# Optimization experiments

Measured on AMD Instinct MI355X. Metric: run time of the kernel, lower is better.

The kernel has to match this reference:

```python
import jax, jax.numpy as jnp
import numpy as np

B, T, S, D, V = 8, 128, 400, 512, 50000
EPS_LN = 1e-6

def setup_inputs() -> dict:
    key = jax.random.key(0)
    ks = jax.random.split(key, 10)
    a = jax.random.uniform(ks[0], (B, T, S), dtype=jnp.float32)
    attn_weights = a / jnp.sum(a, axis=-1, keepdims=True)  # row-stochastic like softmax attention
    return {
        'x': jax.random.normal(ks[1], (B, T, D), dtype=jnp.float32),
        'x_t': jax.random.normal(ks[2], (B, T, D), dtype=jnp.float32),
        'memory': jax.random.normal(ks[3], (B, S, D), dtype=jnp.float32),
        'attn_weights': attn_weights,
        'src': jax.random.randint(ks[4], (B, S), 0, V),
        'norm_a': jnp.ones((D,), jnp.float32),
        'norm_b': jnp.zeros((D,), jnp.float32),
        'proj_w': jax.random.normal(ks[5], (V, D), dtype=jnp.float32) * (1.0 / np.sqrt(D)),
        'proj_b': jnp.zeros((V,), jnp.float32),
        'wh_w': jax.random.normal(ks[6], (1, D), dtype=jnp.float32) * (1.0 / np.sqrt(D)),
        'wh_b': jnp.zeros((1,), jnp.float32),
        'ws_w': jax.random.normal(ks[7], (1, D), dtype=jnp.float32) * (1.0 / np.sqrt(D)),
        'ws_b': jnp.zeros((1,), jnp.float32),
        'wx_w': jax.random.normal(ks[8], (1, D), dtype=jnp.float32) * (1.0 / np.sqrt(D)),
        'wx_b': jnp.zeros((1,), jnp.float32),
        'bptr': jnp.zeros((1, 1), jnp.float32),
    }

def _layer_norm(x, a, b):
    mu = jnp.mean(x, axis=-1, keepdims=True)
    sd = jnp.std(x, axis=-1, keepdims=True)
    return a * (x - mu) / (sd + EPS_LN) + b

def reference(x, x_t, memory, attn_weights, src, norm_a, norm_b, proj_w, proj_b,
              wh_w, wh_b, ws_w, ws_b, wx_w, wx_b, bptr):
    # generation distribution over vocab: [B,T,V]
    dec_dist = jnp.einsum('btd,vd->btv', _layer_norm(x, norm_a, norm_b), proj_w) + proj_b
    # context vector h_t = attn @ memory: [B,T,D]
    h_t = jnp.einsum('bts,bsd->btd', attn_weights, memory)
    # p_gen gate: [B,T,1]
    logits = (jnp.einsum('btd,od->bto', h_t, wh_w) + wh_b
              + jnp.einsum('btd,od->bto', x, ws_w) + ws_b
              + jnp.einsum('btd,od->bto', x_t, wx_w) + wx_b
              + bptr[0, 0])
    p_gen = jax.nn.sigmoid(logits)
    # copy distribution via scatter_add of attention mass onto source token ids
    b_idx = jnp.arange(B)[:, None, None]
    t_idx = jnp.arange(T)[None, :, None]
    v_idx = src[:, None, :]  # broadcast over T -> [B,T,S] index
    enc_attn_dist = jnp.zeros((B, T, V), dtype=dec_dist.dtype).at[b_idx, t_idx, v_idx].add(attn_weights)
    out = jnp.log(p_gen * jax.nn.softmax(dec_dist, axis=-1) + (1.0 - p_gen) * enc_attn_dist + 1e-12)
    return out, p_gen
```

## Files before the change

### kernel.cpp

```cpp
#include <hip/hip_runtime.h>
#include <hip/hip_bf16.h>
#include <cstdint>

#define B_  8
#define T_  128
#define S_  400
#define D_  512
#define V_  50000
#define M_  (B_*T_)
#define NT_ 391
#define EPS_LN 1e-6f

typedef __bf16 bf16x8 __attribute__((ext_vector_type(8)));
typedef float  f32x4  __attribute__((ext_vector_type(4)));
typedef unsigned short u16;
typedef unsigned short u16x8 __attribute__((ext_vector_type(8)));

__device__ __forceinline__ float bf2f(u16 u) {
    union { unsigned i; float f; } c; c.i = ((unsigned)u) << 16; return c.f;
}
__device__ __forceinline__ u16 f2bf(float f) {
    union { float f; unsigned i; } c; c.f = f;
    unsigned i = c.i;
    unsigned r = (i + 0x7FFFu + ((i >> 16) & 1u)) >> 16;
    return (u16)r;
}

__device__ __forceinline__ float bsum(float v, float* sb) {
    #pragma unroll
    for (int o = 32; o; o >>= 1) v += __shfl_xor(v, o);
    __syncthreads();
    if ((threadIdx.x & 63) == 0) sb[threadIdx.x >> 6] = v;
    __syncthreads();
    return sb[0] + sb[1] + sb[2] + sb[3];
}

__global__ void k_mw(const float* __restrict__ mem, const float* __restrict__ wh,
                     float* __restrict__ mw) {
    __shared__ float sb[4];
    int row = blockIdx.x;
    const float* mr = mem + (size_t)row * D_;
    int t = threadIdx.x;
    float2 m2 = *(const float2*)(mr + t * 2);
    float2 w2 = *(const float2*)(wh + t * 2);
    float v = m2.x * w2.x + m2.y * w2.y;
    float tot = bsum(v, sb);
    if (t == 0) mw[row] = tot;
}

__global__ void k_wconv(const float* __restrict__ w, u16* __restrict__ wb) {
    size_t i = ((size_t)blockIdx.x * 256 + threadIdx.x) * 8;
    float4 a = *(const float4*)(w + i);
    float4 b = *(const float4*)(w + i + 4);
    u16x8 o;
    o[0] = f2bf(a.x); o[1] = f2bf(a.y); o[2] = f2bf(a.z); o[3] = f2bf(a.w);
    o[4] = f2bf(b.x); o[5] = f2bf(b.y); o[6] = f2bf(b.z); o[7] = f2bf(b.w);
    *(u16x8*)(wb + i) = o;
}

__global__ void k_rows(const float* __restrict__ x, const float* __restrict__ xt,
                       const float* __restrict__ attn, const float* __restrict__ mw,
                       const float* __restrict__ na, const float* __restrict__ nb,
                       const float* __restrict__ wsw, const float* __restrict__ wxw,
                       const float* __restrict__ whb, const float* __restrict__ wsb,
                       const float* __restrict__ wxb, const float* __restrict__ bp,
                       u16* __restrict__ Ab, float* __restrict__ pgen,
                       float* __restrict__ outp) {
    __shared__ float sb[4];
    int row = blockIdx.x;
    int b = row / T_;
    int tid = threadIdx.x;
    const float* xr  = x  + (size_t)row * D_;
    const float* xtr = xt + (size_t)row * D_;
    float2 xv = *(const float2*)(xr + tid * 2);
    float tsx  = bsum(xv.x + xv.y, sb);
    float tsx2 = bsum(xv.x * xv.x + xv.y * xv.y, sb);
    float mu  = tsx / (float)D_;
    float var = fmaxf(tsx2 / (float)D_ - mu * mu, 0.f);
    float rs  = 1.f / (sqrtf(var) + EPS_LN);
    float2 nav = *(const float2*)(na + tid * 2);
    float2 nbv = *(const float2*)(nb + tid * 2);
    u16 a0 = f2bf(nav.x * (xv.x - mu) * rs + nbv.x);
    u16 a1 = f2bf(nav.y * (xv.y - mu) * rs + nbv.y);
    ((unsigned*)(Ab + (size_t)row * D_))[tid] = (unsigned)a0 | ((unsigned)a1 << 16);
    float2 wsv = *(const float2*)(wsw + tid * 2);
    float2 wxv = *(const float2*)(wxw + tid * 2);
    float2 xtv = *(const float2*)(xtr + tid * 2);
    float dot = xv.x * wsv.x + xv.y * wsv.y + xtv.x * wxv.x + xtv.y * wxv.y;
    if (tid < 200) {
        const float* ar  = attn + (size_t)row * S_;
        const float* mwb = mw + b * S_;
        float2 av = *(const float2*)(ar + tid * 2);
        float2 mv = *(const float2*)(mwb + tid * 2);
        dot += av.x * mv.x + av.y * mv.y;
    }
    float tdot = bsum(dot, sb);
    if (tid == 0) {
        float logit = tdot + whb[0] + wsb[0] + wxb[0] + bp[0];
        float p = 1.f / (1.f + __expf(-logit));
        pgen[row] = p;
        outp[row] = p;
    }
}

__global__ __launch_bounds__(256) void k_gemm(const u16* __restrict__ Ab,
                                              const u16* __restrict__ Wb,
                                              const float* __restrict__ projb,
                                              u16* __restrict__ dec,
                                              float* __restrict__ psum) {
    __shared__ __align__(16) char smem[49152];
    int bid = blockIdx.x;
    int xcd = bid & 7, loc = bid >> 3;
    int wg = xcd * NT_ + loc;
    int mt = wg & 7, nt = wg >> 3;
    int brow = mt * 128, bcol = nt * 128;
    int tid = threadIdx.x, lane = tid & 63, wv = tid >> 6;
    int wm = wv >> 1, wn = wv & 1;
    int kq = lane >> 4, lr = lane & 15;

    size_t aoff[2], boff[2];
    int flatoff[2];
    #pragma unroll
    for (int i = 0; i < 2; ++i) {
        int flat = i * 4096 + tid * 16;
        flatoff[i] = flat;
        int sub = flat >> 10;
        int l   = (flat >> 4) & 63;
        int kq2 = l >> 4, lr2 = l & 15;
        int arow = brow + sub * 16 + lr2;
        int vrow = bcol + sub * 16 + lr2; if (vrow >= V_) vrow = V_ - 1;
        aoff[i] = (size_t)arow * 512 + kq2 * 8;
        boff[i] = (size_t)vrow * 512 + kq2 * 8;
    }

#define STAGE(buf, kt) { \
    char* ab = smem + (buf) * 16384; \
    _Pragma("unroll") \
    for (int i = 0; i < 2; ++i) { \
        __builtin_amdgcn_global_load_lds( \
            (const __attribute__((address_space(1))) unsigned*)(Ab + aoff[i] + (size_t)(kt) * 32), \
            (__attribute__((address_space(3))) unsigned*)(ab + flatoff[i]), 16, 0, 0); \
        __builtin_amdgcn_global_load_lds( \
            (const __attribute__((address_space(1))) unsigned*)(Wb + boff[i] + (size_t)(kt) * 32), \
            (__attribute__((address_space(3))) unsigned*)(ab + 8192 + flatoff[i]), 16, 0, 0); \
    } }

    f32x4 acc[4][4] = {};
    STAGE(0, 0);
    STAGE(1, 1);
    STAGE(2, 2);
    asm volatile("s_waitcnt vmcnt(8)" ::: "memory");
    __builtin_amdgcn_s_barrier();
    __builtin_amdgcn_sched_barrier(0);
    for (int kt = 0; kt < 16; ++kt) {
        int cur = kt % 3;
        const bf16x8* Afp = (const bf16x8*)(smem + cur * 16384);
        const bf16x8* Bfp = (const bf16x8*)(smem + cur * 16384 + 8192);
        bf16x8 af[4], bfr[4];
        #pragma unroll
        for (int m = 0; m < 4; ++m) af[m]  = Afp[(wm * 4 + m) * 64 + lane];
        #pragma unroll
        for (int n = 0; n < 4; ++n) bfr[n] = Bfp[(wn * 4 + n) * 64 + lane];
        #pragma unroll
        for (int m = 0; m < 4; ++m)
            #pragma unroll
            for (int n = 0; n < 4; ++n)
                acc[m][n] = __builtin_amdgcn_mfma_f32_16x16x32_bf16(af[m], bfr[n], acc[m][n], 0, 0, 0);
        __builtin_amdgcn_sched_barrier(0);
        if (kt == 15) break;
        if (kt < 14) { asm volatile("s_waitcnt vmcnt(4)" ::: "memory"); }
        else         { asm volatile("s_waitcnt vmcnt(0)" ::: "memory"); }
        __builtin_amdgcn_s_barrier();
        __builtin_amdgcn_sched_barrier(0);
        if (kt < 13) STAGE(cur, kt + 3);
    }
#undef STAGE
    __syncthreads();

    float pbn[4]; int cvaln[4];
    #pragma unroll
    for (int n = 0; n < 4; ++n) {
        int col = bcol + wn * 64 + n * 16 + lr;
        cvaln[n] = (col < V_);
        pbn[n] = cvaln[n] ? projb[col] : 0.f;
    }
    u16 (*Os)[136] = (u16(*)[136])smem;
    float* ssum = (float*)(smem + 34816);
    #pragma unroll
    for (int m = 0; m < 4; ++m) {
        #pragma unroll
        for (int i = 0; i < 4; ++i) {
            int row128 = wm * 64 + m * 16 + kq * 4 + i;
            float se = 0.f;
            #pragma unroll
            for (int n = 0; n < 4; ++n) {
                float dv = acc[m][n][i] + pbn[n];
                if (cvaln[n]) se += __expf(dv);
                Os[row128][wn * 64 + n * 16 + lr] = f2bf(dv);
            }
            #pragma unroll
            for (int o = 1; o < 16; o <<= 1) se += __shfl_xor(se, o);
            if (lr == 0) ssum[wn * 128 + row128] = se;
        }
    }
    __syncthreads();
    if (tid < 128) {
        psum[(size_t)(brow + tid) * NT_ + nt] = ssum[tid] + ssum[128 + tid];
    }
    #pragma unroll
    for (int j = 0; j < 8; ++j) {
        int row = j * 16 + (tid >> 4);
        int c8 = (tid & 15) * 8;
        int gcol = bcol + c8;
        if (gcol + 8 <= V_) {
            u16x8 v = *(const u16x8*)&Os[row][c8];
            *(u16x8*)(dec + (size_t)(brow + row) * V_ + gcol) = v;
        }
    }
}

__global__ void k_reduce(const float* __restrict__ psum, float* __restrict__ base) {
    __shared__ float sb[4];
    int row = blockIdx.x;
    int t = threadIdx.x;
    const float* ps = psum + (size_t)row * NT_;
    float s = 0.f;
    for (int j = t; j < NT_; j += 256) s += ps[j];
    s = bsum(s, sb);
    if (t == 0) base[row] = __logf(s);
}

__global__ void k_final(const u16* __restrict__ dec, const float* __restrict__ pgen,
                        const float* __restrict__ base, float* __restrict__ out) {
    int row = blockIdx.y;
    int v0 = (blockIdx.x * 256 + threadIdx.x) * 8;
    if (v0 >= V_) return;
    float p  = pgen[row];
    float bs = base[row];
    u16x8 d = *(const u16x8*)(dec + (size_t)row * V_ + v0);
    float4 o0, o1;
    o0.x = __logf(p * __expf(bf2f(d[0]) - bs) + 1e-12f);
    o0.y = __logf(p * __expf(bf2f(d[1]) - bs) + 1e-12f);
    o0.z = __logf(p * __expf(bf2f(d[2]) - bs) + 1e-12f);
    o0.w = __logf(p * __expf(bf2f(d[3]) - bs) + 1e-12f);
    o1.x = __logf(p * __expf(bf2f(d[4]) - bs) + 1e-12f);
    o1.y = __logf(p * __expf(bf2f(d[5]) - bs) + 1e-12f);
    o1.z = __logf(p * __expf(bf2f(d[6]) - bs) + 1e-12f);
    o1.w = __logf(p * __expf(bf2f(d[7]) - bs) + 1e-12f);
    float* op = out + (size_t)row * V_ + v0;
    *(float4*)op = o0;
    *(float4*)(op + 4) = o1;
}

__global__ void k_fix(const int* __restrict__ src, const float* __restrict__ attn,
                      const u16* __restrict__ dec, const float* __restrict__ pgen,
                      const float* __restrict__ base, float* __restrict__ out) {
    __shared__ int   sh_sr[S_];
    __shared__ int   sh_fs[S_];
    __shared__ float sh_enc[S_];
    int b = blockIdx.x >> 7;
    int t = blockIdx.x & 127;
    int tid = threadIdx.x;
    const int* sr = src + b * S_;
    for (int s = tid; s < S_; s += 256) { sh_sr[s] = sr[s]; sh_enc[s] = 0.f; }
    __syncthreads();
    for (int s = tid; s < S_; s += 256) {
        int v = sh_sr[s];
        int f = 0;
        while (sh_sr[f] != v) ++f;
        sh_fs[s] = f;
    }
    __syncthreads();
    int row = b * T_ + t;
    const float* ar = attn + (size_t)row * S_;
    for (int s = tid; s < S_; s += 256)
        atomicAdd(&sh_enc[sh_fs[s]], ar[s]);
    __syncthreads();
    float p  = pgen[row];
    float bs = base[row];
    for (int s = tid; s < S_; s += 256) {
        if (sh_fs[s] == s) {
            int v = sh_sr[s];
            float d = bf2f(dec[(size_t)row * V_ + v]);
            out[(size_t)row * V_ + v] =
                __logf(p * __expf(d - bs) + (1.f - p) * sh_enc[s] + 1e-12f);
        }
    }
}

extern "C" void kernel_launch(void* const* d_in, const int* in_sizes, int n_in,
                              void* d_out, int out_size, void* d_ws, size_t ws_size,
                              hipStream_t stream) {
    const float* x    = (const float*)d_in[0];
    const float* xt   = (const float*)d_in[1];
    const float* mem  = (const float*)d_in[2];
    const float* attn = (const float*)d_in[3];
    const int*   src  = (const int*)d_in[4];
    const float* na   = (const float*)d_in[5];
    const float* nb   = (const float*)d_in[6];
    const float* pw   = (const float*)d_in[7];
    const float* pb   = (const float*)d_in[8];
    const float* whw  = (const float*)d_in[9];
    const float* whb  = (const float*)d_in[10];
    const float* wsw  = (const float*)d_in[11];
    const float* wsb  = (const float*)d_in[12];
    const float* wxw  = (const float*)d_in[13];
    const float* wxb  = (const float*)d_in[14];
    const float* bp   = (const float*)d_in[15];

    char* ws = (char*)d_ws;
    u16*   Wb   = (u16*)(ws + 0);
    u16*   Ab   = (u16*)(ws + 51200000);
    u16*   dec  = (u16*)(ws + 52248576);
    float* psum = (float*)(ws + 154648576);
    float* mw   = (float*)(ws + 156250112);
    float* pgen = (float*)(ws + 156262912);
    float* base = (float*)(ws + 156267008);
    float* out  = (float*)d_out;
    float* outp = out + (size_t)M_ * V_;

    k_mw    <<<B_ * S_, 256, 0, stream>>>(mem, whw, mw);
    k_wconv <<<12500, 256, 0, stream>>>(pw, Wb);
    k_rows  <<<M_, 256, 0, stream>>>(x, xt, attn, mw, na, nb, wsw, wxw,
                                     whb, wsb, wxb, bp, Ab, pgen, outp);
    k_gemm  <<<3128, 256, 0, stream>>>(Ab, Wb, pb, dec, psum);
    k_reduce<<<M_, 256, 0, stream>>>(psum, base);
    k_final <<<dim3(25, M_), 256, 0, stream>>>(dec, pgen, base, out);
    k_fix   <<<B_ * T_, 256, 0, stream>>>(src, attn, dec, pgen, base, out);
}
```

Baseline: 269.0 us.

## Enlarge vocab GEMM tile to 256x256 with 512-thread blocks

The projection GEMM moves from 128x128 tiles with 4 waves to 256x256 tiles with 8 waves, each wave owning a 128x64 sub-tile. This raises operand reuse and halves the number of partial softmax sums per row. Shared memory grows to 96KB, taken as dynamic shared memory, and the epilogue writes its output in two 128-row halves through shared memory. The change risks higher register pressure from 32 accumulators per wave, lower occupancy, and a serialized epilogue in which only half the waves work in each phase.

```diff
diff --git a/kernel.cpp b/kernel.cpp
--- a/kernel.cpp
+++ b/kernel.cpp
@@ -8,7 +8,7 @@
 #define D_  512
 #define V_  50000
 #define M_  (B_*T_)
-#define NT_ 391
+#define NTC 196
 #define EPS_LN 1e-6f
 
 typedef __bf16 bf16x8 __attribute__((ext_vector_type(8)));
@@ -103,66 +103,66 @@
     }
 }
 
-__global__ __launch_bounds__(256) void k_gemm(const u16* __restrict__ Ab,
-                                              const u16* __restrict__ Wb,
-                                              const float* __restrict__ projb,
-                                              u16* __restrict__ dec,
-                                              float* __restrict__ psum) {
-    __shared__ __align__(16) char smem[49152];
+__global__ __launch_bounds__(512, 2) void k_gemm(const u16* __restrict__ Ab,
+                                                 const u16* __restrict__ Wb,
+                                                 const float* __restrict__ projb,
+                                                 u16* __restrict__ dec,
+                                                 float* __restrict__ psum) {
+    extern __shared__ __align__(16) char smem[];
     int bid = blockIdx.x;
     int xcd = bid & 7, loc = bid >> 3;
-    int wg = xcd * NT_ + loc;
-    int mt = wg & 7, nt = wg >> 3;
-    int brow = mt * 128, bcol = nt * 128;
+    int wg = xcd * 98 + loc;
+    int mt = wg & 3, nt = wg >> 2;
+    int brow = mt * 256, bcol = nt * 256;
     int tid = threadIdx.x, lane = tid & 63, wv = tid >> 6;
-    int wm = wv >> 1, wn = wv & 1;
+    int wm = wv >> 2, wn = wv & 3;
     int kq = lane >> 4, lr = lane & 15;
 
-    size_t aoff[2], boff[2];
-    int flatoff[2];
+    size_t aglob[2], bglob[2];
+    int flatA[2];
     #pragma unroll
     for (int i = 0; i < 2; ++i) {
-        int flat = i * 4096 + tid * 16;
-        flatoff[i] = flat;
+        int flat = i * 8192 + tid * 16;
+        flatA[i] = flat;
         int sub = flat >> 10;
         int l   = (flat >> 4) & 63;
         int kq2 = l >> 4, lr2 = l & 15;
         int arow = brow + sub * 16 + lr2;
         int vrow = bcol + sub * 16 + lr2; if (vrow >= V_) vrow = V_ - 1;
-        aoff[i] = (size_t)arow * 512 + kq2 * 8;
-        boff[i] = (size_t)vrow * 512 + kq2 * 8;
+        aglob[i] = (size_t)arow * 512 + kq2 * 8;
+        bglob[i] = (size_t)vrow * 512 + kq2 * 8;
     }
 
 #define STAGE(buf, kt) { \
-    char* ab = smem + (buf) * 16384; \
+    char* ab = smem + (buf) * 32768; \
     _Pragma("unroll") \
     for (int i = 0; i < 2; ++i) { \
         __builtin_amdgcn_global_load_lds( \
-            (const __attribute__((address_space(1))) unsigned*)(Ab + aoff[i] + (size_t)(kt) * 32), \
-            (__attribute__((address_space(3))) unsigned*)(ab + flatoff[i]), 16, 0, 0); \
+            (const __attribute__((address_space(1))) unsigned*)(Ab + aglob[i] + (size_t)(kt) * 32), \
+            (__attribute__((address_space(3))) unsigned*)(ab + flatA[i]), 16, 0, 0); \
         __builtin_amdgcn_global_load_lds( \
-            (const __attribute__((address_space(1))) unsigned*)(Wb + boff[i] + (size_t)(kt) * 32), \
-            (__attribute__((address_space(3))) unsigned*)(ab + 8192 + flatoff[i]), 16, 0, 0); \
+            (const __attribute__((address_space(1))) unsigned*)(Wb + bglob[i] + (size_t)(kt) * 32), \
+            (__attribute__((address_space(3))) unsigned*)(ab + 16384 + flatA[i]), 16, 0, 0); \
     } }
 
-    f32x4 acc[4][4] = {};
+    f32x4 acc[8][4] = {};
     STAGE(0, 0);
     STAGE(1, 1);
     STAGE(2, 2);
     asm volatile("s_waitcnt vmcnt(8)" ::: "memory");
     __builtin_amdgcn_s_barrier();
     __builtin_amdgcn_sched_barrier(0);
+    int cur = 0;
     for (int kt = 0; kt < 16; ++kt) {
-        int cur = kt % 3;
-        const bf16x8* Afp = (const bf16x8*)(smem + cur * 16384);
-        const bf16x8* Bfp = (const bf16x8*)(smem + cur * 16384 + 8192);
-        bf16x8 af[4], bfr[4];
+        const bf16x8* Afp = (const bf16x8*)(smem + cur * 32768);
+        const bf16x8* Bfp = (const bf16x8*)(smem + cur * 32768 + 16384);
+        bf16x8 af[8], bfr[4];
         #pragma unroll
-        for (int m = 0; m < 4; ++m) af[m]  = Afp[(wm * 4 + m) * 64 + lane];
+        for (int m = 0; m < 8; ++m) af[m]  = Afp[(wm * 8 + m) * 64 + lane];
         #pragma unroll
         for (int n = 0; n < 4; ++n) bfr[n] = Bfp[(wn * 4 + n) * 64 + lane];
         #pragma unroll
-        for (int m = 0; m < 4; ++m)
+        for (int m = 0; m < 8; ++m)
             #pragma unroll
             for (int n = 0; n < 4; ++n)
                 acc[m][n] = __builtin_amdgcn_mfma_f32_16x16x32_bf16(af[m], bfr[n], acc[m][n], 0, 0, 0);
@@ -173,6 +173,7 @@
         __builtin_amdgcn_s_barrier();
         __builtin_amdgcn_sched_barrier(0);
         if (kt < 13) STAGE(cur, kt + 3);
+        cur = (cur == 2) ? 0 : cur + 1;
     }
 #undef STAGE
     __syncthreads();
@@ -184,38 +185,44 @@
         cvaln[n] = (col < V_);
         pbn[n] = cvaln[n] ? projb[col] : 0.f;
     }
-    u16 (*Os)[136] = (u16(*)[136])smem;
-    float* ssum = (float*)(smem + 34816);
-    #pragma unroll
-    for (int m = 0; m < 4; ++m) {
+    u16 (*Os)[264] = (u16(*)[264])smem;
+    float* ssum = (float*)(smem + 67584);
+    #pragma unroll 1
+    for (int h = 0; h < 2; ++h) {
+        if (wm == h) {
+            #pragma unroll
+            for (int m = 0; m < 8; ++m) {
+                #pragma unroll
+                for (int i = 0; i < 4; ++i) {
+                    int row128 = m * 16 + kq * 4 + i;
+                    float se = 0.f;
+                    #pragma unroll
+                    for (int n = 0; n < 4; ++n) {
+                        float dv = acc[m][n][i] + pbn[n];
+                        if (cvaln[n]) se += __expf(dv);
+                        Os[row128][wn * 64 + n * 16 + lr] = f2bf(dv);
+                    }
+                    #pragma unroll
+                    for (int o = 1; o < 16; o <<= 1) se += __shfl_xor(se, o);
+                    if (lr == 0) ssum[wn * 128 + row128] = se;
+                }
+            }
+        }
+        __syncthreads();
+        if (tid < 128) {
+            psum[(size_t)(brow + h * 128 + tid) * NTC + nt] =
+                ssum[tid] + ssum[128 + tid] + ssum[256 + tid] + ssum[384 + tid];
+        }
         #pragma unroll
-        for (int i = 0; i < 4; ++i) {
-            int row128 = wm * 64 + m * 16 + kq * 4 + i;
-            float se = 0.f;
-            #pragma unroll
-            for (int n = 0; n < 4; ++n) {
-                float dv = acc[m][n][i] + pbn[n];
-                if (cvaln[n]) se += __expf(dv);
-                Os[row128][wn * 64 + n * 16 + lr] = f2bf(dv);
+        for (int j = 0; j < 8; ++j) {
+            int row = j * 16 + (tid >> 5);
+            int c8 = (tid & 31) * 8;
+            if (bcol + c8 + 8 <= V_) {
+                u16x8 v = *(const u16x8*)&Os[row][c8];
+                *(u16x8*)(dec + (size_t)(brow + h * 128 + row) * V_ + bcol + c8) = v;
             }
-            #pragma unroll
-            for (int o = 1; o < 16; o <<= 1) se += __shfl_xor(se, o);
-            if (lr == 0) ssum[wn * 128 + row128] = se;
         }
-    }
-    __syncthreads();
-    if (tid < 128) {
-        psum[(size_t)(brow + tid) * NT_ + nt] = ssum[tid] + ssum[128 + tid];
-    }
-    #pragma unroll
-    for (int j = 0; j < 8; ++j) {
-        int row = j * 16 + (tid >> 4);
-        int c8 = (tid & 15) * 8;
-        int gcol = bcol + c8;
-        if (gcol + 8 <= V_) {
-            u16x8 v = *(const u16x8*)&Os[row][c8];
-            *(u16x8*)(dec + (size_t)(brow + row) * V_ + gcol) = v;
-        }
+        __syncthreads();
     }
 }
 
@@ -223,9 +230,9 @@
     __shared__ float sb[4];
     int row = blockIdx.x;
     int t = threadIdx.x;
-    const float* ps = psum + (size_t)row * NT_;
+    const float* ps = psum + (size_t)row * NTC;
     float s = 0.f;
-    for (int j = t; j < NT_; j += 256) s += ps[j];
+    for (int j = t; j < NTC; j += 256) s += ps[j];
     s = bsum(s, sb);
     if (t == 0) base[row] = __logf(s);
 }
@@ -313,17 +320,20 @@
     u16*   Ab   = (u16*)(ws + 51200000);
     u16*   dec  = (u16*)(ws + 52248576);
     float* psum = (float*)(ws + 154648576);
-    float* mw   = (float*)(ws + 156250112);
-    float* pgen = (float*)(ws + 156262912);
-    float* base = (float*)(ws + 156267008);
+    float* mw   = (float*)(ws + 155451392);
+    float* pgen = (float*)(ws + 155464192);
+    float* base = (float*)(ws + 155468288);
     float* out  = (float*)d_out;
     float* outp = out + (size_t)M_ * V_;
+
+    (void)hipFuncSetAttribute(reinterpret_cast<const void*>(k_gemm),
+                              hipFuncAttributeMaxDynamicSharedMemorySize, 98304);
 
     k_mw    <<<B_ * S_, 256, 0, stream>>>(mem, whw, mw);
     k_wconv <<<12500, 256, 0, stream>>>(pw, Wb);
     k_rows  <<<M_, 256, 0, stream>>>(x, xt, attn, mw, na, nb, wsw, wxw,
                                      whb, wsb, wxb, bp, Ab, pgen, outp);
-    k_gemm  <<<3128, 256, 0, stream>>>(Ab, Wb, pb, dec, psum);
+    k_gemm  <<<784, 512, 98304, stream>>>(Ab, Wb, pb, dec, psum);
     k_reduce<<<M_, 256, 0, stream>>>(psum, base);
     k_final <<<dim3(25, M_), 256, 0, stream>>>(dec, pgen, base, out);
     k_fix   <<<B_ * T_, 256, 0, stream>>>(src, attn, dec, pgen, base, out);
```

Result: slower. 281.1 us (+4.5%).
